# Performance work log

Hardware: AMD Instinct MI355X
Metric: run time of the kernel (lower is better)

## Reference

```python
import jax, jax.numpy as jnp
import numpy as np

B, V, D, H, E = 512, 128, 256, 4, 2
Dh = D // H

def setup_inputs() -> dict:
    key = jax.random.key(0)
    k = jax.random.split(key, 8)
    x = jax.random.normal(k[0], (B, V, D), dtype=jnp.float32)
    adj = jax.random.randint(k[1], (V, V), 0, 2, dtype=jnp.int32)
    adj = adj.at[jnp.arange(V), jnp.arange(V)].set(1)  # self loops so no empty columns for real nodes
    edge_attr = jax.random.normal(k[2], (V, V, E), dtype=jnp.float32)
    mask = jax.random.bernoulli(k[3], 0.1, (B, V))  # True = padded view
    # learned params (torch Linear: y = x @ W.T)
    W = jax.random.normal(k[4], (D, D), dtype=jnp.float32) / np.sqrt(D)
    a = jax.random.normal(k[5], (2 * Dh,), dtype=jnp.float32) / np.sqrt(2 * Dh)  # attn.weight flattened
    Ew = jax.random.normal(k[6], (H, E), dtype=jnp.float32) / np.sqrt(E)  # edge_proj.weight
    return {"x": x, "adj": adj, "edge_attr": edge_attr, "mask": mask, "W": W, "a": a, "Ew": Ew}

def reference(x, adj, edge_attr, mask, W, a, Ew):
    Bv, Vv, Dv = x.shape
    Hh = Ew.shape[0]
    Dhh = Dv // Hh
    Wx = (x @ W.T).reshape(Bv, Vv, Hh, Dhh)                 # [B,V,H,Dh]
    a_src, a_dst = a[:Dhh], a[Dhh:]
    s_src = jnp.einsum('bvhd,d->bvh', Wx, a_src)             # a^T[Wh_i ; .]
    s_dst = jnp.einsum('bvhd,d->bvh', Wx, a_dst)             # a^T[. ; Wh_j]
    ef = jnp.einsum('ije,he->ijh', edge_attr, Ew)            # [V,V,H]
    e = s_src[:, :, None, :] + s_dst[:, None, :, :] + ef[None]  # [B,i,j,H]
    e = jnp.where(e >= 0, e, 0.2 * e)                        # leaky_relu(0.2)
    valid = (adj.astype(bool))[None, :, :, None] & (~mask)[:, :, None, None] & (~mask)[:, None, :, None]
    e = jnp.where(valid, e, -jnp.inf)
    # softmax over source dim i (axis=1), safe for all-masked columns (-> 0, like nan_to_num)
    m = jnp.max(e, axis=1, keepdims=True)
    m = jnp.where(jnp.isfinite(m), m, 0.0)
    p = jnp.where(valid, jnp.exp(e - m), 0.0)
    denom = jnp.sum(p, axis=1, keepdims=True)
    alpha = p / jnp.where(denom == 0, 1.0, denom)            # [B,i,j,H]
    h = jnp.einsum('bijh,bihd->bjhd', alpha, Wx).reshape(Bv, Vv, Dv)
    h = jax.nn.elu(h)
    return jnp.where(mask[:, :, None], 0.0, h)
```

## Files before the change

kernel.cpp:

```cpp
#include <hip/hip_runtime.h>
#include <cmath>

#define BB 512
#define VV 128
#define DD 256
#define HH 4
#define DHH 64

typedef unsigned short u16;
typedef __attribute__((ext_vector_type(8))) short bf16x8;
typedef __attribute__((ext_vector_type(4))) short bf16x4;
typedef __attribute__((ext_vector_type(4))) float f32x4;

__device__ __forceinline__ u16 f2bf(float f) {
    unsigned u = __builtin_bit_cast(unsigned, f);
    u = (u + 0x7fffu + ((u >> 16) & 1u)) >> 16;
    return (u16)u;
}
__device__ __forceinline__ unsigned pk2(float a, float b) {
    return (unsigned)f2bf(a) | ((unsigned)f2bf(b) << 16);
}

__global__ void k_ef(const float* __restrict__ ea, const float* __restrict__ Ew,
                     const int* __restrict__ adj, float* __restrict__ efm) {
    int idx = blockIdx.x * 256 + threadIdx.x;
    int hh = idx >> 14, ij = idx & 16383;
    float v = -INFINITY;
    if (adj[ij])
        v = fmaf(ea[ij * 2 + 1], Ew[hh * 2 + 1], ea[ij * 2] * Ew[hh * 2]);
    efm[idx] = v;
}

__global__ __launch_bounds__(256, 2) void k_fused(
    const float* __restrict__ x, const float* __restrict__ Wm,
    const float* __restrict__ a, const float* __restrict__ efm,
    const int* __restrict__ mask, float* __restrict__ out) {
    __shared__ u16 WxL[128 * 136];
    __shared__ u16 scratch[128 * 136];
    __shared__ float ssl[256], sdl[256], red[256], rden[128];
    __shared__ int mkl[128];

    u16* As = scratch;
    u16* Bs = scratch + 128 * 40;
    u16* alT = scratch;

    const int t = threadIdx.x;
    const int b = blockIdx.x, hp = blockIdx.y;
    const int w = t >> 6, L = t & 63;
    const int wr = w >> 1, wc = w & 1;
    const int lr = L & 15, lg = L >> 4;

    if (t < 128) mkl[t] = mask[b * VV + t];

    const int row = t >> 1, seg = t & 1;
    const float* xs = x  + ((size_t)b * VV + row) * DD + seg * 16;
    const float* ws = Wm + ((size_t)(hp * 128 + row)) * DD + seg * 16;
    u16* adst = As + row * 40 + seg * 16;
    u16* bdst = Bs + row * 40 + seg * 16;

    f32x4 acc[4][4];
    #pragma unroll
    for (int i = 0; i < 4; ++i)
        #pragma unroll
        for (int j = 0; j < 4; ++j) acc[i][j] = (f32x4){0.f, 0.f, 0.f, 0.f};

    float4 px[4], pw[4];
    #pragma unroll
    for (int q = 0; q < 4; ++q) {
        px[q] = *(const float4*)(xs + q * 4);
        pw[q] = *(const float4*)(ws + q * 4);
    }

    for (int ks = 0; ks < 8; ++ks) {
        bf16x8 va, vb, qa, qb;
        unsigned* vap = (unsigned*)&va; unsigned* vbp = (unsigned*)&vb;
        unsigned* qap = (unsigned*)&qa; unsigned* qbp = (unsigned*)&qb;
        vap[0] = pk2(px[0].x, px[0].y); vap[1] = pk2(px[0].z, px[0].w);
        vap[2] = pk2(px[1].x, px[1].y); vap[3] = pk2(px[1].z, px[1].w);
        vbp[0] = pk2(px[2].x, px[2].y); vbp[1] = pk2(px[2].z, px[2].w);
        vbp[2] = pk2(px[3].x, px[3].y); vbp[3] = pk2(px[3].z, px[3].w);
        qap[0] = pk2(pw[0].x, pw[0].y); qap[1] = pk2(pw[0].z, pw[0].w);
        qap[2] = pk2(pw[1].x, pw[1].y); qap[3] = pk2(pw[1].z, pw[1].w);
        qbp[0] = pk2(pw[2].x, pw[2].y); qbp[1] = pk2(pw[2].z, pw[2].w);
        qbp[2] = pk2(pw[3].x, pw[3].y); qbp[3] = pk2(pw[3].z, pw[3].w);
        *(bf16x8*)adst       = va;
        *(bf16x8*)(adst + 8) = vb;
        *(bf16x8*)bdst       = qa;
        *(bf16x8*)(bdst + 8) = qb;
        __syncthreads();
        if (ks < 7) {
            #pragma unroll
            for (int q = 0; q < 4; ++q) {
                px[q] = *(const float4*)(xs + (ks + 1) * 32 + q * 4);
                pw[q] = *(const float4*)(ws + (ks + 1) * 32 + q * 4);
            }
        }
        bf16x8 af[4], bfr[4];
        #pragma unroll
        for (int mi = 0; mi < 4; ++mi)
            af[mi] = *(const bf16x8*)&As[(wr * 64 + mi * 16 + lr) * 40 + lg * 8];
        #pragma unroll
        for (int ni = 0; ni < 4; ++ni)
            bfr[ni] = *(const bf16x8*)&Bs[(wc * 64 + ni * 16 + lr) * 40 + lg * 8];
        #pragma unroll
        for (int mi = 0; mi < 4; ++mi)
            #pragma unroll
            for (int ni = 0; ni < 4; ++ni)
                acc[mi][ni] = __builtin_amdgcn_mfma_f32_16x16x32_bf16(
                    af[mi], bfr[ni], acc[mi][ni], 0, 0, 0);
        __syncthreads();
    }

    float as_[4], ad_[4];
    #pragma unroll
    for (int ni = 0; ni < 4; ++ni) {
        as_[ni] = a[ni * 16 + lr];
        ad_[ni] = a[64 + ni * 16 + lr];
    }
    float ps[16], pd[16];
    #pragma unroll
    for (int k = 0; k < 16; ++k) { ps[k] = 0.f; pd[k] = 0.f; }
    #pragma unroll
    for (int mi = 0; mi < 4; ++mi) {
        #pragma unroll
        for (int ni = 0; ni < 4; ++ni) {
            const int c  = wc * 64 + ni * 16 + lr;
            const int vb = wr * 64 + mi * 16 + lg * 4;
            bf16x4 o;
            #pragma unroll
            for (int r = 0; r < 4; ++r) {
                float v = acc[mi][ni][r];
                o[r] = (short)f2bf(v);
                ps[mi * 4 + r] = fmaf(v, as_[ni], ps[mi * 4 + r]);
                pd[mi * 4 + r] = fmaf(v, ad_[ni], pd[mi * 4 + r]);
            }
            *(bf16x4*)&WxL[c * 136 + vb] = o;
        }
    }
    #pragma unroll
    for (int k = 0; k < 16; ++k) {
        #pragma unroll
        for (int m = 1; m < 16; m <<= 1) {
            ps[k] += __shfl_xor(ps[k], m);
            pd[k] += __shfl_xor(pd[k], m);
        }
    }
    if (lr == 0) {
        #pragma unroll
        for (int mi = 0; mi < 4; ++mi)
            #pragma unroll
            for (int r = 0; r < 4; ++r) {
                int v = wr * 64 + mi * 16 + lg * 4 + r;
                bool mk = mkl[v] != 0;
                ssl[wc * 128 + v] = mk ? -INFINITY : ps[mi * 4 + r];
                sdl[wc * 128 + v] = mk ? -INFINITY : pd[mi * 4 + r];
            }
    }
    __syncthreads();

    const int j = t & 127, half = t >> 7;
    for (int hl = 0; hl < 2; ++hl) {
        const int h = hp * 2 + hl;
        const float sdj = sdl[hl * 128 + j];
        const float* efh = efm + ((size_t)h * VV + half * 64) * VV + j;
        u16* alrow = alT + j * 136 + half * 64;
        float psum = 0.f;
        for (int i8 = 0; i8 < 64; i8 += 8) {
            bf16x8 pk;
            #pragma unroll
            for (int u = 0; u < 8; ++u) {
                float e = ssl[hl * 128 + half * 64 + i8 + u] + sdj
                        + efh[(size_t)(i8 + u) * VV];
                e = e >= 0.f ? e : 0.2f * e;
                float p = __expf(e);
                psum += p;
                pk[u] = (short)f2bf(p);
            }
            *(bf16x8*)(alrow + i8) = pk;
        }
        red[half * 128 + j] = psum;
        __syncthreads();
        if (half == 0) {
            float s = red[j] + red[128 + j];
            rden[j] = s > 0.f ? 1.f / s : 0.f;
        }
        __syncthreads();

        f32x4 acc2[2][4];
        #pragma unroll
        for (int mi = 0; mi < 2; ++mi)
            #pragma unroll
            for (int ni = 0; ni < 4; ++ni) acc2[mi][ni] = (f32x4){0.f, 0.f, 0.f, 0.f};
        #pragma unroll
        for (int ks = 0; ks < 4; ++ks) {
            const int kk = ks * 32 + lg * 8;
            bf16x8 bfr2[4];
            #pragma unroll
            for (int ni = 0; ni < 4; ++ni)
                bfr2[ni] = *(const bf16x8*)&WxL[(hl * 64 + ni * 16 + lr) * 136 + kk];
            #pragma unroll
            for (int mi = 0; mi < 2; ++mi) {
                bf16x8 af2 = *(const bf16x8*)&alT[(w * 32 + mi * 16 + lr) * 136 + kk];
                #pragma unroll
                for (int ni = 0; ni < 4; ++ni)
                    acc2[mi][ni] = __builtin_amdgcn_mfma_f32_16x16x32_bf16(
                        af2, bfr2[ni], acc2[mi][ni], 0, 0, 0);
            }
        }
        #pragma unroll
        for (int mi = 0; mi < 2; ++mi)
            #pragma unroll
            for (int ni = 0; ni < 4; ++ni) {
                const int dcol = ni * 16 + lr;
                const int jb   = w * 32 + mi * 16 + lg * 4;
                float* op = out + ((size_t)b * VV + jb) * DD + h * DHH + dcol;
                #pragma unroll
                for (int r = 0; r < 4; ++r) {
                    float v = acc2[mi][ni][r] * rden[jb + r];
                    v = v > 0.f ? v : expm1f(v);
                    op[(size_t)r * DD] = v;
                }
            }
        __syncthreads();
    }
}

extern "C" void kernel_launch(void* const* d_in, const int* in_sizes, int n_in,
                              void* d_out, int out_size, void* d_ws, size_t ws_size,
                              hipStream_t stream) {
    const float* x    = (const float*)d_in[0];
    const int*   adj  = (const int*)d_in[1];
    const float* ea   = (const float*)d_in[2];
    const int*   mask = (const int*)d_in[3];
    const float* Wm   = (const float*)d_in[4];
    const float* a    = (const float*)d_in[5];
    const float* Ew   = (const float*)d_in[6];
    float* out = (float*)d_out;

    float* efm = (float*)d_ws;

    k_ef<<<HH * VV * VV / 256, 256, 0, stream>>>(ea, Ew, adj, efm);
    k_fused<<<dim3(BB, 2), 256, 0, stream>>>(x, Wm, a, efm, mask, out);
}
```

Baseline: 166.3 us.

## Compute attention probabilities directly in MFMA registers and halve shared memory

The edge-feature table is now stored transposed so each lane can read contiguous source-node values for its target column with vector loads. The softmax numerators are computed straight into the MFMA A-operand registers instead of going through a shared-memory alpha buffer. The column sums are reduced with wave shuffles, which removes a shared reduction and two barriers per head. Dropping the alpha buffer halves shared memory, and launch bounds are raised to allow 4 blocks per CU. The cost is more register pressure and a more complex k_ef that transposes through a shared tile.

```diff
diff --git a/kernel.cpp b/kernel.cpp
--- a/kernel.cpp
+++ b/kernel.cpp
@@ -21,28 +21,42 @@
     return (unsigned)f2bf(a) | ((unsigned)f2bf(b) << 16);
 }
 
-__global__ void k_ef(const float* __restrict__ ea, const float* __restrict__ Ew,
-                     const int* __restrict__ adj, float* __restrict__ efm) {
-    int idx = blockIdx.x * 256 + threadIdx.x;
-    int hh = idx >> 14, ij = idx & 16383;
-    float v = -INFINITY;
-    if (adj[ij])
-        v = fmaf(ea[ij * 2 + 1], Ew[hh * 2 + 1], ea[ij * 2] * Ew[hh * 2]);
-    efm[idx] = v;
-}
-
-__global__ __launch_bounds__(256, 2) void k_fused(
+__global__ __launch_bounds__(256) void k_ef(const float* __restrict__ ea,
+                                            const float* __restrict__ Ew,
+                                            const int* __restrict__ adj,
+                                            float* __restrict__ efmT) {
+    __shared__ float tile[128 * 33];
+    const int t = threadIdx.x;
+    const int h = blockIdx.x, jt = blockIdx.y;
+    const int tj = t & 31, ti = t >> 5;
+    const float e0 = Ew[h * 2], e1 = Ew[h * 2 + 1];
+    for (int k = 0; k < 16; ++k) {
+        int i  = k * 8 + ti;
+        int ij = i * VV + jt * 32 + tj;
+        float v = -INFINITY;
+        if (adj[ij]) v = fmaf(ea[ij * 2 + 1], e1, ea[ij * 2] * e0);
+        tile[i * 33 + tj] = v;
+    }
+    __syncthreads();
+    const int i2 = t & 127, jh = t >> 7;
+    float* dst = efmT + (size_t)h * VV * VV;
+    for (int m = 0; m < 16; ++m) {
+        int j = m * 2 + jh;
+        dst[(size_t)(jt * 32 + j) * VV + i2] = tile[i2 * 33 + j];
+    }
+}
+
+__global__ __launch_bounds__(256, 4) void k_fused(
     const float* __restrict__ x, const float* __restrict__ Wm,
-    const float* __restrict__ a, const float* __restrict__ efm,
+    const float* __restrict__ a, const float* __restrict__ efmT,
     const int* __restrict__ mask, float* __restrict__ out) {
-    __shared__ u16 WxL[128 * 136];
-    __shared__ u16 scratch[128 * 136];
-    __shared__ float ssl[256], sdl[256], red[256], rden[128];
+    __shared__ u16 ubuf[128 * 136];
+    __shared__ float ssl[256], sdl[256], rden[2][128];
     __shared__ int mkl[128];
 
-    u16* As = scratch;
-    u16* Bs = scratch + 128 * 40;
-    u16* alT = scratch;
+    u16* As  = ubuf;
+    u16* Bs  = ubuf + 128 * 40;
+    u16* WxL = ubuf;
 
     const int t = threadIdx.x;
     const int b = blockIdx.x, hp = blockIdx.y;
@@ -158,33 +172,48 @@
     }
     __syncthreads();
 
-    const int j = t & 127, half = t >> 7;
+    const int j0 = w * 32 + lr;
     for (int hl = 0; hl < 2; ++hl) {
         const int h = hp * 2 + hl;
-        const float sdj = sdl[hl * 128 + j];
-        const float* efh = efm + ((size_t)h * VV + half * 64) * VV + j;
-        u16* alrow = alT + j * 136 + half * 64;
-        float psum = 0.f;
-        for (int i8 = 0; i8 < 64; i8 += 8) {
-            bf16x8 pk;
+        const float sdj0 = sdl[hl * 128 + j0];
+        const float sdj1 = sdl[hl * 128 + j0 + 16];
+        const float* ef0 = efmT + ((size_t)h * VV + j0) * VV;
+        const float* ef1 = ef0 + 16 * VV;
+        bf16x8 af2[2][4];
+        float ps0 = 0.f, ps1 = 0.f;
+        #pragma unroll
+        for (int ks = 0; ks < 4; ++ks) {
+            const int i0 = ks * 32 + lg * 8;
+            float sv[8], ev0[8], ev1[8];
+            *(float4*)&sv[0]  = *(const float4*)&ssl[hl * 128 + i0];
+            *(float4*)&sv[4]  = *(const float4*)&ssl[hl * 128 + i0 + 4];
+            *(float4*)&ev0[0] = *(const float4*)(ef0 + i0);
+            *(float4*)&ev0[4] = *(const float4*)(ef0 + i0 + 4);
+            *(float4*)&ev1[0] = *(const float4*)(ef1 + i0);
+            *(float4*)&ev1[4] = *(const float4*)(ef1 + i0 + 4);
+            float p0[8], p1[8];
             #pragma unroll
             for (int u = 0; u < 8; ++u) {
-                float e = ssl[hl * 128 + half * 64 + i8 + u] + sdj
-                        + efh[(size_t)(i8 + u) * VV];
-                e = e >= 0.f ? e : 0.2f * e;
-                float p = __expf(e);
-                psum += p;
-                pk[u] = (short)f2bf(p);
-            }
-            *(bf16x8*)(alrow + i8) = pk;
-        }
-        red[half * 128 + j] = psum;
-        __syncthreads();
-        if (half == 0) {
-            float s = red[j] + red[128 + j];
-            rden[j] = s > 0.f ? 1.f / s : 0.f;
-        }
-        __syncthreads();
+                float e0 = sv[u] + sdj0 + ev0[u];
+                float e1 = sv[u] + sdj1 + ev1[u];
+                e0 = fmaxf(e0, 0.2f * e0);
+                e1 = fmaxf(e1, 0.2f * e1);
+                p0[u] = __expf(e0); ps0 += p0[u];
+                p1[u] = __expf(e1); ps1 += p1[u];
+            }
+            unsigned* a0 = (unsigned*)&af2[0][ks];
+            unsigned* a1 = (unsigned*)&af2[1][ks];
+            a0[0] = pk2(p0[0], p0[1]); a0[1] = pk2(p0[2], p0[3]);
+            a0[2] = pk2(p0[4], p0[5]); a0[3] = pk2(p0[6], p0[7]);
+            a1[0] = pk2(p1[0], p1[1]); a1[1] = pk2(p1[2], p1[3]);
+            a1[2] = pk2(p1[4], p1[5]); a1[3] = pk2(p1[6], p1[7]);
+        }
+        ps0 += __shfl_xor(ps0, 16); ps0 += __shfl_xor(ps0, 32);
+        ps1 += __shfl_xor(ps1, 16); ps1 += __shfl_xor(ps1, 32);
+        if (lg == 0) {
+            rden[hl][j0]      = ps0 > 0.f ? 1.f / ps0 : 0.f;
+            rden[hl][j0 + 16] = ps1 > 0.f ? 1.f / ps1 : 0.f;
+        }
 
         f32x4 acc2[2][4];
         #pragma unroll
@@ -194,19 +223,17 @@
         #pragma unroll
         for (int ks = 0; ks < 4; ++ks) {
             const int kk = ks * 32 + lg * 8;
-            bf16x8 bfr2[4];
-            #pragma unroll
-            for (int ni = 0; ni < 4; ++ni)
-                bfr2[ni] = *(const bf16x8*)&WxL[(hl * 64 + ni * 16 + lr) * 136 + kk];
-            #pragma unroll
-            for (int mi = 0; mi < 2; ++mi) {
-                bf16x8 af2 = *(const bf16x8*)&alT[(w * 32 + mi * 16 + lr) * 136 + kk];
-                #pragma unroll
-                for (int ni = 0; ni < 4; ++ni)
-                    acc2[mi][ni] = __builtin_amdgcn_mfma_f32_16x16x32_bf16(
-                        af2, bfr2[ni], acc2[mi][ni], 0, 0, 0);
-            }
-        }
+            #pragma unroll
+            for (int ni = 0; ni < 4; ++ni) {
+                bf16x8 bf2 = *(const bf16x8*)&WxL[(hl * 64 + ni * 16 + lr) * 136 + kk];
+                acc2[0][ni] = __builtin_amdgcn_mfma_f32_16x16x32_bf16(
+                    af2[0][ks], bf2, acc2[0][ni], 0, 0, 0);
+                acc2[1][ni] = __builtin_amdgcn_mfma_f32_16x16x32_bf16(
+                    af2[1][ks], bf2, acc2[1][ni], 0, 0, 0);
+            }
+        }
+        __syncthreads();
+
         #pragma unroll
         for (int mi = 0; mi < 2; ++mi)
             #pragma unroll
@@ -216,12 +243,11 @@
                 float* op = out + ((size_t)b * VV + jb) * DD + h * DHH + dcol;
                 #pragma unroll
                 for (int r = 0; r < 4; ++r) {
-                    float v = acc2[mi][ni][r] * rden[jb + r];
+                    float v = acc2[mi][ni][r] * rden[hl][jb + r];
                     v = v > 0.f ? v : expm1f(v);
                     op[(size_t)r * DD] = v;
                 }
             }
-        __syncthreads();
     }
 }
 
@@ -237,8 +263,8 @@
     const float* Ew   = (const float*)d_in[6];
     float* out = (float*)d_out;
 
-    float* efm = (float*)d_ws;
-
-    k_ef<<<HH * VV * VV / 256, 256, 0, stream>>>(ea, Ew, adj, efm);
-    k_fused<<<dim3(BB, 2), 256, 0, stream>>>(x, Wm, a, efm, mask, out);
-}
+    float* efmT = (float*)d_ws;
+
+    k_ef<<<dim3(HH, VV / 32), 256, 0, stream>>>(ea, Ew, adj, efmT);
+    k_fused<<<dim3(BB, 2), 256, 0, stream>>>(x, Wm, a, efmT, mask, out);
+}
```

New measurement: 167.5 us. Within noise of the previous version (+0.7%).
